# Performance work log

Hardware: AMD Instinct MI355X
Metric: run time of the kernel (lower is better)

The kernel has to match this reference:

```python
import jax, jax.numpy as jnp
import numpy as np
from jax import lax


def setup_inputs() -> dict:
    key = jax.random.key(0)
    k1, k2 = jax.random.split(key)
    X = jax.random.normal(k1, (4, 32, 512, 512), dtype=jnp.float32)
    kernel = jax.random.uniform(k2, (5, 5), dtype=jnp.float32)  # torch.rand equivalent
    return {"X": X, "kernel": kernel, "stride": 1, "padding": 2}


def reference(X, kernel, stride, padding):
    # Original module: zero-pad, unfold k x k patches with given stride, and
    # compute sum(patch * kernel) for every (batch, channel, row, col) -- i.e.
    # a per-channel 2D correlation with a single shared [k, k] kernel.
    # Fold channels into the batch dim so one single-channel correlation
    # covers all of them (no cross-channel mixing in the original).
    B, C, H, W = X.shape
    k = kernel.shape[0]
    Xf = X.reshape(B * C, 1, H, W)
    out = lax.conv_general_dilated(
        Xf,
        kernel[None, None, :, :],  # OIHW = [1, 1, k, k]
        window_strides=(stride, stride),
        padding=[(padding, padding), (padding, padding)],
        dimension_numbers=("NCHW", "OIHW", "NCHW"),
    )  # lax conv is correlation (no kernel flip), matching the torch math
    _, _, Ho, Wo = out.shape
    return out.reshape(B, C, Ho, Wo)
```

## Files before the change

kernel.cpp:

```cpp
#include <hip/hip_runtime.h>

#define H 512
#define W 512
#define K 5
#define PAD 2
#define RPT 4
#define XPT 4

typedef float vf4 __attribute__((ext_vector_type(4)));

__global__ __launch_bounds__(256) void conv5x5_kernel(
    const float* __restrict__ X, const float* __restrict__ ker,
    float* __restrict__ out)
{
    const int tx  = threadIdx.x;
    const int xb  = (blockIdx.x * 64 + tx) * XPT;
    const int y0  = blockIdx.y * (4 * RPT) + threadIdx.y * RPT;
    const int img = blockIdx.z;

    const float* Xp = X   + (size_t)img * H * W;
    float*       Op = out + (size_t)img * H * W;

    float kk[K][K];
    #pragma unroll
    for (int i = 0; i < K; ++i)
        #pragma unroll
        for (int j = 0; j < K; ++j)
            kk[i][j] = ker[i * K + j];

    float acc[RPT][XPT];
    #pragma unroll
    for (int o = 0; o < RPT; ++o)
        #pragma unroll
        for (int j = 0; j < XPT; ++j)
            acc[o][j] = 0.f;

    const int q  = xb >> 2;
    const int qL = (q == 0) ? 0 : q - 1;
    const int qR = (q == W / 4 - 1) ? q : q + 1;
    const float mLo = (q == 0) ? 0.f : 1.f;
    const float mHi = (q == W / 4 - 1) ? 0.f : 1.f;

    #pragma unroll
    for (int r = 0; r < RPT + K - 1; ++r) {
        const int yr = y0 - PAD + r;
        vf4 Lv = {0.f, 0.f, 0.f, 0.f};
        vf4 Mv = {0.f, 0.f, 0.f, 0.f};
        vf4 Rv = {0.f, 0.f, 0.f, 0.f};
        if (yr >= 0 && yr < H) {
            const vf4* rp = (const vf4*)(Xp + (size_t)yr * W);
            Lv = rp[qL];
            Mv = rp[q];
            Rv = rp[qR];
        }
        float v[8];
        v[0] = Lv.z * mLo;  v[1] = Lv.w * mLo;
        v[2] = Mv.x;  v[3] = Mv.y;  v[4] = Mv.z;  v[5] = Mv.w;
        v[6] = Rv.x * mHi;  v[7] = Rv.y * mHi;

        #pragma unroll
        for (int o = 0; o < RPT; ++o) {
            const int kr = r - o;
            if (kr >= 0 && kr < K) {
                #pragma unroll
                for (int c = 0; c < K; ++c)
                    #pragma unroll
                    for (int j = 0; j < XPT; ++j)
                        acc[o][j] = fmaf(v[j + c], kk[kr][c], acc[o][j]);
            }
        }
    }

    #pragma unroll
    for (int o = 0; o < RPT; ++o) {
        vf4 st = {acc[o][0], acc[o][1], acc[o][2], acc[o][3]};
        __builtin_nontemporal_store(st, (vf4*)(Op + (size_t)(y0 + o) * W + xb));
    }
}

extern "C" void kernel_launch(void* const* d_in, const int* in_sizes, int n_in,
                              void* d_out, int out_size, void* d_ws, size_t ws_size,
                              hipStream_t stream) {
    const float* X   = (const float*)d_in[0];
    const float* ker = (const float*)d_in[1];
    float* out = (float*)d_out;

    dim3 block(64, 4, 1);
    dim3 grid(W / (64 * XPT), H / (4 * RPT), 4 * 32);
    hipLaunchKernelGGL(conv5x5_kernel, grid, block, 0, stream, X, ker, out);
}
```

Baseline: 231.5 us.

## Stream 16 output rows per thread with rotating 5-row accumulator ring

```diff
diff --git a/kernel.cpp b/kernel.cpp
--- a/kernel.cpp
+++ b/kernel.cpp
@@ -4,7 +4,7 @@
 #define W 512
 #define K 5
 #define PAD 2
-#define RPT 4
+#define ROWS 16
 #define XPT 4
 
 typedef float vf4 __attribute__((ext_vector_type(4)));
@@ -15,7 +15,7 @@
 {
     const int tx  = threadIdx.x;
     const int xb  = (blockIdx.x * 64 + tx) * XPT;
-    const int y0  = blockIdx.y * (4 * RPT) + threadIdx.y * RPT;
+    const int y0  = blockIdx.y * (4 * ROWS) + threadIdx.y * ROWS;
     const int img = blockIdx.z;
 
     const float* Xp = X   + (size_t)img * H * W;
@@ -28,21 +28,21 @@
         for (int j = 0; j < K; ++j)
             kk[i][j] = ker[i * K + j];
 
-    float acc[RPT][XPT];
-    #pragma unroll
-    for (int o = 0; o < RPT; ++o)
-        #pragma unroll
-        for (int j = 0; j < XPT; ++j)
-            acc[o][j] = 0.f;
-
     const int q  = xb >> 2;
     const int qL = (q == 0) ? 0 : q - 1;
     const int qR = (q == W / 4 - 1) ? q : q + 1;
     const float mLo = (q == 0) ? 0.f : 1.f;
     const float mHi = (q == W / 4 - 1) ? 0.f : 1.f;
 
+    float acc[K][XPT];
     #pragma unroll
-    for (int r = 0; r < RPT + K - 1; ++r) {
+    for (int p = 0; p < K; ++p)
+        #pragma unroll
+        for (int j = 0; j < XPT; ++j)
+            acc[p][j] = 0.f;
+
+    #pragma unroll
+    for (int r = 0; r < ROWS + K - 1; ++r) {
         const int yr = y0 - PAD + r;
         vf4 Lv = {0.f, 0.f, 0.f, 0.f};
         vf4 Mv = {0.f, 0.f, 0.f, 0.f};
@@ -59,22 +59,27 @@
         v[6] = Rv.x * mHi;  v[7] = Rv.y * mHi;
 
         #pragma unroll
-        for (int o = 0; o < RPT; ++o) {
-            const int kr = r - o;
-            if (kr >= 0 && kr < K) {
+        for (int kr = 0; kr < K; ++kr) {
+            const int o = r - kr;
+            if (o >= 0 && o < ROWS) {
+                const int pa = o % K;
                 #pragma unroll
                 for (int c = 0; c < K; ++c)
                     #pragma unroll
                     for (int j = 0; j < XPT; ++j)
-                        acc[o][j] = fmaf(v[j + c], kk[kr][c], acc[o][j]);
+                        acc[pa][j] = fmaf(v[j + c], kk[kr][c], acc[pa][j]);
             }
         }
-    }
 
-    #pragma unroll
-    for (int o = 0; o < RPT; ++o) {
-        vf4 st = {acc[o][0], acc[o][1], acc[o][2], acc[o][3]};
-        __builtin_nontemporal_store(st, (vf4*)(Op + (size_t)(y0 + o) * W + xb));
+        if (r >= K - 1) {
+            const int o  = r - (K - 1);
+            const int pa = o % K;
+            vf4 st = {acc[pa][0], acc[pa][1], acc[pa][2], acc[pa][3]};
+            __builtin_nontemporal_store(st, (vf4*)(Op + (size_t)(y0 + o) * W + xb));
+            #pragma unroll
+            for (int j = 0; j < XPT; ++j)
+                acc[pa][j] = 0.f;
+        }
     }
 }
 
@@ -86,6 +91,6 @@
     float* out = (float*)d_out;
 
     dim3 block(64, 4, 1);
-    dim3 grid(W / (64 * XPT), H / (4 * RPT), 4 * 32);
+    dim3 grid(W / (64 * XPT), H / (4 * ROWS), 4 * 32);
     hipLaunchKernelGGL(conv5x5_kernel, grid, block, 0, stream, X, ker, out);
 }
```

New measurement: 236.8 us. 2.3% more time.

## Stage input row tiles in LDS via direct global-to-LDS loads

Applied to the files above, without the earlier changes.

```diff
diff --git a/kernel.cpp b/kernel.cpp
--- a/kernel.cpp
+++ b/kernel.cpp
@@ -4,22 +4,40 @@
 #define W 512
 #define K 5
 #define PAD 2
-#define RPT 4
+#define TROWS 8
+#define IROWS (TROWS + K - 1)
 #define XPT 4
+#define NCHUNK (IROWS * W * 4 / 16)
+#define CPT (NCHUNK / 256)
 
 typedef float vf4 __attribute__((ext_vector_type(4)));
 
-__global__ __launch_bounds__(256) void conv5x5_kernel(
+__global__ __launch_bounds__(256, 6) void conv5x5_kernel(
     const float* __restrict__ X, const float* __restrict__ ker,
     float* __restrict__ out)
 {
+    __shared__ float tile[IROWS][W];
+
     const int tx  = threadIdx.x;
-    const int xb  = (blockIdx.x * 64 + tx) * XPT;
-    const int y0  = blockIdx.y * (4 * RPT) + threadIdx.y * RPT;
-    const int img = blockIdx.z;
+    const int y0  = blockIdx.x * TROWS;
+    const int img = blockIdx.y;
 
     const float* Xp = X   + (size_t)img * H * W;
     float*       Op = out + (size_t)img * H * W;
+
+    #pragma unroll
+    for (int k = 0; k < CPT; ++k) {
+        const int c   = tx + 256 * k;
+        const int rr  = c >> 7;
+        const int c16 = c & 127;
+        int yr = y0 - PAD + rr;
+        yr = yr < 0 ? 0 : (yr > H - 1 ? H - 1 : yr);
+        const float* src = Xp + (size_t)yr * W + c16 * 4;
+        __builtin_amdgcn_global_load_lds(
+            (const __attribute__((address_space(1))) void*)src,
+            (__attribute__((address_space(3))) void*)&tile[rr][c16 * 4],
+            16, 0, 0);
+    }
 
     float kk[K][K];
     #pragma unroll
@@ -28,38 +46,42 @@
         for (int j = 0; j < K; ++j)
             kk[i][j] = ker[i * K + j];
 
-    float acc[RPT][XPT];
+    __syncthreads();
+
+    const int q  = tx & 127;
+    const int ty = tx >> 7;
+    const int qL = (q == 0)   ? 0 : q - 1;
+    const int qR = (q == 127) ? q : q + 1;
+    const float mLo = (q == 0)   ? 0.f : 1.f;
+    const float mHi = (q == 127) ? 0.f : 1.f;
+    const int rbase = ty * 4;
+
+    float acc[4][XPT];
     #pragma unroll
-    for (int o = 0; o < RPT; ++o)
+    for (int o = 0; o < 4; ++o)
         #pragma unroll
         for (int j = 0; j < XPT; ++j)
             acc[o][j] = 0.f;
 
-    const int q  = xb >> 2;
-    const int qL = (q == 0) ? 0 : q - 1;
-    const int qR = (q == W / 4 - 1) ? q : q + 1;
-    const float mLo = (q == 0) ? 0.f : 1.f;
-    const float mHi = (q == W / 4 - 1) ? 0.f : 1.f;
-
     #pragma unroll
-    for (int r = 0; r < RPT + K - 1; ++r) {
-        const int yr = y0 - PAD + r;
-        vf4 Lv = {0.f, 0.f, 0.f, 0.f};
-        vf4 Mv = {0.f, 0.f, 0.f, 0.f};
-        vf4 Rv = {0.f, 0.f, 0.f, 0.f};
-        if (yr >= 0 && yr < H) {
-            const vf4* rp = (const vf4*)(Xp + (size_t)yr * W);
-            Lv = rp[qL];
-            Mv = rp[q];
-            Rv = rp[qR];
-        }
+    for (int r = 0; r < 8; ++r) {
+        const int lr = rbase + r;
+        const int yr = y0 - PAD + lr;
+        const float mR = (yr >= 0 && yr < H) ? 1.f : 0.f;
+        const vf4* rp = (const vf4*)&tile[lr][0];
+        const vf4 Lv = rp[qL];
+        const vf4 Mv = rp[q];
+        const vf4 Rv = rp[qR];
+        const float mA = mLo * mR;
+        const float mC = mHi * mR;
         float v[8];
-        v[0] = Lv.z * mLo;  v[1] = Lv.w * mLo;
-        v[2] = Mv.x;  v[3] = Mv.y;  v[4] = Mv.z;  v[5] = Mv.w;
-        v[6] = Rv.x * mHi;  v[7] = Rv.y * mHi;
+        v[0] = Lv.z * mA;  v[1] = Lv.w * mA;
+        v[2] = Mv.x * mR;  v[3] = Mv.y * mR;
+        v[4] = Mv.z * mR;  v[5] = Mv.w * mR;
+        v[6] = Rv.x * mC;  v[7] = Rv.y * mC;
 
         #pragma unroll
-        for (int o = 0; o < RPT; ++o) {
+        for (int o = 0; o < 4; ++o) {
             const int kr = r - o;
             if (kr >= 0 && kr < K) {
                 #pragma unroll
@@ -72,9 +94,10 @@
     }
 
     #pragma unroll
-    for (int o = 0; o < RPT; ++o) {
+    for (int o = 0; o < 4; ++o) {
         vf4 st = {acc[o][0], acc[o][1], acc[o][2], acc[o][3]};
-        __builtin_nontemporal_store(st, (vf4*)(Op + (size_t)(y0 + o) * W + xb));
+        __builtin_nontemporal_store(
+            st, (vf4*)(Op + (size_t)(y0 + rbase + o) * W + q * XPT));
     }
 }
 
@@ -85,7 +108,7 @@
     const float* ker = (const float*)d_in[1];
     float* out = (float*)d_out;
 
-    dim3 block(64, 4, 1);
-    dim3 grid(W / (64 * XPT), H / (4 * RPT), 4 * 32);
+    dim3 block(256, 1, 1);
+    dim3 grid(H / TROWS, 4 * 32, 1);
     hipLaunchKernelGGL(conv5x5_kernel, grid, block, 0, stream, X, ker, out);
 }
```

Result: slower. 249.1 us (+7.6%).
